# Performance work log

Hardware: AMD Instinct MI355X
Metric: run time of the kernel (lower is better)

## Reference

```python
import jax, jax.numpy as jnp
import numpy as np


def gru_cell(inp, h, wi, wh, bi, bh):
    # torch nn.GRU cell math: gates ordered (r, z, n)
    gi = inp @ wi.T + bi          # [3H]
    gh = h @ wh.T + bh            # [3H]
    ir, iz, inn = jnp.split(gi, 3, axis=-1)
    hr, hz, hn = jnp.split(gh, 3, axis=-1)
    r = jax.nn.sigmoid(ir + hr)
    z = jax.nn.sigmoid(iz + hz)
    n = jnp.tanh(inn + r * hn)
    return (1.0 - z) * n + z * h


def setup_inputs() -> dict:
    key = jax.random.key(0)
    C, L = 1024, 2048  # input_size / hidden_size, sequence length
    ks = jax.random.split(key, 11)
    x = jax.random.normal(ks[0], (1, L, C), jnp.float32)
    # attention: Linear(2C, 1), weight ~ N(0, 0.01), bias = -1 (per module init)
    attn_w = jax.random.normal(ks[1], (1, 2 * C), jnp.float32) * 0.01
    attn_b = jnp.full((1,), -1.0, jnp.float32)
    # GRU default torch init: U(-1/sqrt(H), 1/sqrt(H))
    s = 1.0 / np.sqrt(C).astype(np.float32)
    u = lambda k, shape: jax.random.uniform(k, shape, jnp.float32, -s, s)
    w_ih0 = u(ks[2], (3 * C, C)); w_hh0 = u(ks[3], (3 * C, C))
    b_ih0 = u(ks[4], (3 * C,));   b_hh0 = u(ks[5], (3 * C,))
    w_ih1 = u(ks[6], (3 * C, C)); w_hh1 = u(ks[7], (3 * C, C))
    b_ih1 = u(ks[8], (3 * C,));   b_hh1 = u(ks[9], (3 * C,))
    return {"x": x, "attn_w": attn_w, "attn_b": attn_b,
            "w_ih0": w_ih0, "w_hh0": w_hh0, "b_ih0": b_ih0, "b_hh0": b_hh0,
            "w_ih1": w_ih1, "w_hh1": w_hh1, "b_ih1": b_ih1, "b_hh1": b_hh1,
            "lengths": L}


def reference(x, attn_w, attn_b, w_ih0, w_hh0, b_ih0, b_hh0,
              w_ih1, w_hh1, b_ih1, b_hh1, lengths):
    x0 = x[0]                     # [L, C]; batch must be 1
    L, C = x0.shape
    dt = x.dtype

    def step(carry, _):
        out, h0, h1 = carry       # out: [C], h0/h1: [C]
        # attention: score each timestep against previous output
        concated = jnp.concatenate(
            [jnp.broadcast_to(out, (L, C)), x0], axis=1)  # [L, 2C]
        logits = concated @ attn_w.T + attn_b             # [L, 1]
        a = jax.nn.softmax(logits, axis=0)                # softmax over L
        av = jnp.sum(a * x0, axis=0)                      # [C] context vector
        # 2-layer GRU, one timestep
        h0n = gru_cell(av, h0, w_ih0, w_hh0, b_ih0, b_hh0)
        h1n = gru_cell(h0n, h1, w_ih1, w_hh1, b_ih1, b_hh1)
        return (h1n, h0n, h1n), h1n

    init = (jnp.zeros((C,), dt), jnp.zeros((C,), dt), jnp.zeros((C,), dt))
    (_, h0, h1), outs = jax.lax.scan(step, init, None, length=lengths)
    outputs = outs[None]                                  # [1, L, C]
    previous_state = jnp.stack([h0, h1])[:, None, :]      # [2, 1, C]
    return outputs, previous_state
```

## Files before the change

### kernel.cpp

```cpp
#include <hip/hip_runtime.h>
#include <math.h>

#define CC 1024
#define LL 2048
#define NWG 256
#define NT 256

typedef float f4 __attribute__((ext_vector_type(4)));
typedef unsigned u4 __attribute__((ext_vector_type(4)));

#define H1_BASE 4096
#define PKT_PAR 2048
#define WS_FLAGS 8192
#define WS_REL 16384
#define WS_LOGITS 16448
#define WS_AV (WS_LOGITS + LL)
#define WS_MEMSET_BYTES ((WS_REL + 64) * 4)

__device__ __forceinline__ float aload(const float* p) {
  return __hip_atomic_load(p, __ATOMIC_RELAXED, __HIP_MEMORY_SCOPE_AGENT);
}
__device__ __forceinline__ void astore(float* p, float v) {
  __hip_atomic_store(p, v, __ATOMIC_RELAXED, __HIP_MEMORY_SCOPE_AGENT);
}
__device__ __forceinline__ float sigm(float x) { return 1.0f / (1.0f + __expf(-x)); }
__device__ __forceinline__ float tanh_(float x) { return 2.0f / (1.0f + __expf(-2.0f * x)) - 1.0f; }
__device__ __forceinline__ float dot4(f4 a, f4 b) {
  return fmaf(a.x, b.x, fmaf(a.y, b.y, fmaf(a.z, b.z, a.w * b.w)));
}

__device__ __forceinline__ u4 ld16v(const unsigned* p) {
  u4 r;
  asm volatile("global_load_dwordx4 %0, %1, off sc0 sc1" : "=v"(r) : "v"(p) : "memory");
  return r;
}
__device__ __forceinline__ void vm0() { asm volatile("s_waitcnt vmcnt(0)" ::: "memory"); }

__device__ __forceinline__ void pub8(unsigned* p, unsigned val, unsigned tag) {
  unsigned long long pk = (unsigned long long)val | ((unsigned long long)tag << 32);
  (void)__hip_atomic_exchange((unsigned long long*)p, pk, __ATOMIC_RELAXED,
                              __HIP_MEMORY_SCOPE_AGENT);
}

__device__ __forceinline__ void gbar(unsigned* ws_u, unsigned epoch) {
  __syncthreads();
  if (blockIdx.x == 0) {
    const int i = threadIdx.x;
    if (i > 0 && i < NWG) {
      unsigned* slot = ws_u + WS_FLAGS + i * 32;
      while (__hip_atomic_load(slot, __ATOMIC_RELAXED, __HIP_MEMORY_SCOPE_AGENT) < epoch) {
      }
      (void)__hip_atomic_load(slot, __ATOMIC_ACQUIRE, __HIP_MEMORY_SCOPE_AGENT);
    }
    __syncthreads();
    if (i == 0)
      __hip_atomic_store(ws_u + WS_REL, epoch, __ATOMIC_RELEASE, __HIP_MEMORY_SCOPE_AGENT);
    __syncthreads();
  } else {
    if (threadIdx.x == 0) {
      __hip_atomic_store(ws_u + WS_FLAGS + blockIdx.x * 32, epoch, __ATOMIC_RELEASE,
                         __HIP_MEMORY_SCOPE_AGENT);
      unsigned* rel = ws_u + WS_REL;
      while (__hip_atomic_load(rel, __ATOMIC_RELAXED, __HIP_MEMORY_SCOPE_AGENT) < epoch) {
      }
      (void)__hip_atomic_load(rel, __ATOMIC_ACQUIRE, __HIP_MEMORY_SCOPE_AGENT);
    }
    __syncthreads();
  }
}

#define PIN12                                                                        \
  asm volatile("" : "+v"(Wa[0]), "+v"(Wa[1]), "+v"(Wa[2]), "+v"(Wa[3]), "+v"(Wa[4]), \
                    "+v"(Wa[5]), "+v"(Wa[6]), "+v"(Wa[7]), "+v"(Wa[8]), "+v"(Wa[9]), \
                    "+v"(Wa[10]), "+v"(Wa[11]))

__global__ __launch_bounds__(NT, 1) void decoder_kernel(
    const float* __restrict__ x, const float* __restrict__ attn_w,
    const float* __restrict__ w_ih0, const float* __restrict__ w_hh0,
    const float* __restrict__ b_ih0, const float* __restrict__ b_hh0,
    const float* __restrict__ w_ih1, const float* __restrict__ w_hh1,
    const float* __restrict__ b_ih1, const float* __restrict__ b_hh1,
    float* __restrict__ out, float* __restrict__ ws) {
  const int g = blockIdx.x;
  const int tid = threadIdx.x;
  const int lane = tid & 63;
  const int w = tid >> 6;
  const int eg = 4 * g + w;

  unsigned* ws_u = (unsigned*)ws;

  extern __shared__ float wcb[];
  __shared__ __align__(16) float h0s[CC];
  __shared__ __align__(16) float h1s[CC];
  __shared__ float cgi0[12], cbh0[12], cbh1[12], cbi1[12];
  __shared__ float red[NT];

  {
    const float* w2 = attn_w + CC;
#pragma unroll
    for (int s = 0; s < 2; ++s) {
      int t = 8 * g + 2 * w + s;
      const float* xr = x + (size_t)t * CC;
      float p = 0.f;
#pragma unroll
      for (int k = 0; k < 4; ++k) {
        f4 xa = *(const f4*)(xr + 256 * k + 4 * lane);
        f4 wa = *(const f4*)(w2 + 256 * k + 4 * lane);
        p += dot4(xa, wa);
      }
#pragma unroll
      for (int off = 32; off; off >>= 1) p += __shfl_xor(p, off, 64);
      if (lane == 0) astore(ws + WS_LOGITS + t, p);
    }
  }
  gbar(ws_u, 1);

  {
    float myl[8];
#pragma unroll
    for (int s = 0; s < 8; ++s) myl[s] = aload(ws + WS_LOGITS + tid + 256 * s);
    float lm = myl[0];
#pragma unroll
    for (int s = 1; s < 8; ++s) lm = fmaxf(lm, myl[s]);
    red[tid] = lm;
    __syncthreads();
    for (int stp = 128; stp; stp >>= 1) {
      if (tid < stp) red[tid] = fmaxf(red[tid], red[tid + stp]);
      __syncthreads();
    }
    float m = red[0];
    __syncthreads();
    float myw[8];
    float ls = 0.f;
#pragma unroll
    for (int s = 0; s < 8; ++s) {
      myw[s] = __expf(myl[s] - m);
      ls += myw[s];
    }
    red[tid] = ls;
    __syncthreads();
    for (int stp = 128; stp; stp >>= 1) {
      if (tid < stp) red[tid] += red[tid + stp];
      __syncthreads();
    }
    float invZ = 1.0f / red[0];
    __syncthreads();
    float acc[4] = {0.f, 0.f, 0.f, 0.f};
#pragma unroll
    for (int s = 0; s < 8; ++s) {
      int t = tid + 256 * s;
      f4 xa = *(const f4*)(x + (size_t)t * CC + 4 * g);
      acc[0] = fmaf(myw[s], xa.x, acc[0]);
      acc[1] = fmaf(myw[s], xa.y, acc[1]);
      acc[2] = fmaf(myw[s], xa.z, acc[2]);
      acc[3] = fmaf(myw[s], xa.w, acc[3]);
    }
    for (int i = 0; i < 4; ++i) {
      red[tid] = acc[i];
      __syncthreads();
      for (int stp = 128; stp; stp >>= 1) {
        if (tid < stp) red[tid] += red[tid + stp];
        __syncthreads();
      }
      if (tid == 0) astore(ws + WS_AV + 4 * g + i, red[0] * invZ);
      __syncthreads();
    }
  }
  gbar(ws_u, 2);

#pragma unroll
  for (int i = 0; i < 4; ++i) h0s[4 * tid + i] = aload(ws + WS_AV + 4 * tid + i);
  __syncthreads();
  {
    f4 hc[4];
#pragma unroll
    for (int k = 0; k < 4; ++k) hc[k] = *(const f4*)&h0s[256 * k + 4 * lane];
#pragma unroll
    for (int jj = 0; jj < 3; ++jj) {
      int j = 3 * w + jj;
      int gate = j >> 2, e = j & 3;
      int row = gate * CC + 4 * g + e;
      const float* wr = w_ih0 + (size_t)row * CC;
      float p = 0.f;
#pragma unroll
      for (int k = 0; k < 4; ++k) p += dot4(*(const f4*)(wr + 256 * k + 4 * lane), hc[k]);
#pragma unroll
      for (int off = 32; off; off >>= 1) p += __shfl_xor(p, off, 64);
      if (lane == 0) cgi0[j] = p + b_ih0[row];
    }
  }
  if (tid < 12) {
    int gate = tid >> 2, e = tid & 3;
    int row = gate * CC + 4 * g + e;
    cbh0[tid] = b_hh0[row];
    cbh1[tid] = b_hh1[row];
    cbi1[tid] = b_ih1[row];
  }

  f4 Wa[12];
#pragma unroll
  for (int G = 0; G < 3; ++G) {
    const float* wr = w_hh0 + ((size_t)(G * CC + eg) << 10);
#pragma unroll
    for (int k = 0; k < 4; ++k) Wa[G * 4 + k] = *(const f4*)(wr + 256 * k + 4 * lane);
  }

#pragma unroll
  for (int j = 0; j < 24; ++j) {
    int ww = j / 6, r = j % 6;
    int G = r % 3;
    const float* src = (r < 3 ? w_ih1 : w_hh1) + ((size_t)(G * CC + 4 * g + ww) << 10);
    *(f4*)&wcb[(j << 10) + 4 * tid] = *(const f4*)(src + 4 * tid);
  }
#pragma unroll
  for (int i = 0; i < 4; ++i) {
    h0s[4 * tid + i] = 0.f;
    h1s[4 * tid + i] = 0.f;
  }
  __syncthreads();

  float h0last = 0.f;
  u4 pd0a, pd0b, pd1a, pd1b;
  const float* wr6 = wcb + (w * 6) * 1024;

  for (int tau = 0; tau <= LL; ++tau) {
    PIN12;
    if (tau > 0) {
      const unsigned ut = (unsigned)tau;
      const unsigned* p0 = ws_u + (tau & 1) * PKT_PAR + 8 * tid;
      vm0();
      while (pd0a.y != ut || pd0a.w != ut || pd0b.y != ut || pd0b.w != ut) {
        pd0a = ld16v(p0);
        pd0b = ld16v(p0 + 4);
        vm0();
      }
      h0s[4 * tid + 0] = __uint_as_float(pd0a.x);
      h0s[4 * tid + 1] = __uint_as_float(pd0a.z);
      h0s[4 * tid + 2] = __uint_as_float(pd0b.x);
      h0s[4 * tid + 3] = __uint_as_float(pd0b.z);
      const unsigned* p1 = ws_u + H1_BASE + (tau & 1) * PKT_PAR + 8 * tid;
      pd1a = ld16v(p1);
      pd1b = ld16v(p1 + 4);
    }
    __syncthreads();

    float h0new = 0.f;
    if (tau < LL) {
      f4 hc0[4];
#pragma unroll
      for (int k = 0; k < 4; ++k) hc0[k] = *(const f4*)&h0s[256 * k + 4 * lane];
      float pA[3];
#pragma unroll
      for (int G = 0; G < 3; ++G) {
        float p = 0.f;
#pragma unroll
        for (int k = 0; k < 4; ++k) p += dot4(Wa[G * 4 + k], hc0[k]);
        pA[G] = p;
      }
#pragma unroll
      for (int off = 32; off; off >>= 1) {
#pragma unroll
        for (int i = 0; i < 3; ++i) pA[i] += __shfl_xor(pA[i], off, 64);
      }
      float h0prev = h0s[eg];
      float r0 = sigm(cgi0[w] + pA[0] + cbh0[w]);
      float z0 = sigm(cgi0[4 + w] + pA[1] + cbh0[4 + w]);
      float n0 = tanh_(cgi0[8 + w] + r0 * (pA[2] + cbh0[8 + w]));
      h0new = (1.f - z0) * n0 + z0 * h0prev;
      if (tau == LL - 1) h0last = h0new;
      if (lane == 0)
        pub8(ws_u + ((tau + 1) & 1) * PKT_PAR + 2 * eg, __float_as_uint(h0new),
             (unsigned)(tau + 1));
    }

    if (tau > 0) {
      const unsigned ut = (unsigned)tau;
      const unsigned* p1 = ws_u + H1_BASE + (tau & 1) * PKT_PAR + 8 * tid;
      vm0();
      while (pd1a.y != ut || pd1a.w != ut || pd1b.y != ut || pd1b.w != ut) {
        pd1a = ld16v(p1);
        pd1b = ld16v(p1 + 4);
        vm0();
      }
      h1s[4 * tid + 0] = __uint_as_float(pd1a.x);
      h1s[4 * tid + 1] = __uint_as_float(pd1a.z);
      h1s[4 * tid + 2] = __uint_as_float(pd1b.x);
      h1s[4 * tid + 3] = __uint_as_float(pd1b.z);
    }
    __syncthreads();

    if (tau >= 1) {
      f4 hc0[4], hc1[4];
#pragma unroll
      for (int k = 0; k < 4; ++k) {
        hc0[k] = *(const f4*)&h0s[256 * k + 4 * lane];
        hc1[k] = *(const f4*)&h1s[256 * k + 4 * lane];
      }
      float pC[3], pB[3];
#pragma unroll
      for (int G = 0; G < 3; ++G) {
        float pc = 0.f, pb = 0.f;
#pragma unroll
        for (int k = 0; k < 4; ++k) {
          int off = 256 * k + 4 * lane;
          pc += dot4(*(const f4*)&wr6[G * 1024 + off], hc0[k]);
          pb += dot4(*(const f4*)&wr6[(3 + G) * 1024 + off], hc1[k]);
        }
        pC[G] = pc;
        pB[G] = pb;
      }
#pragma unroll
      for (int off = 32; off; off >>= 1) {
#pragma unroll
        for (int i = 0; i < 3; ++i) {
          pC[i] += __shfl_xor(pC[i], off, 64);
          pB[i] += __shfl_xor(pB[i], off, 64);
        }
      }
      float h1prev = h1s[eg];
      float r1 = sigm(pC[0] + cbi1[w] + pB[0] + cbh1[w]);
      float z1 = sigm(pC[1] + cbi1[4 + w] + pB[1] + cbh1[4 + w]);
      float n1 = tanh_(pC[2] + cbi1[8 + w] + r1 * (pB[2] + cbh1[8 + w]));
      float h1new = (1.f - z1) * n1 + z1 * h1prev;
      if (lane == 0) {
        if (tau < LL)
          pub8(ws_u + H1_BASE + ((tau + 1) & 1) * PKT_PAR + 2 * eg,
               __float_as_uint(h1new), (unsigned)(tau + 1));
        out[(size_t)(tau - 1) * CC + eg] = h1new;
        if (tau == LL) {
          out[(size_t)LL * CC + eg] = h0last;
          out[(size_t)LL * CC + CC + eg] = h1new;
        }
      }
    } else if (lane == 0) {
      pub8(ws_u + H1_BASE + 1 * PKT_PAR + 2 * eg, 0u, 1u);
    }

    if (tau < LL) {
      const unsigned* np = ws_u + ((tau + 1) & 1) * PKT_PAR + 8 * tid;
      pd0a = ld16v(np);
      pd0b = ld16v(np + 4);
    }
    __syncthreads();
  }
}

extern "C" void kernel_launch(void* const* d_in, const int* in_sizes, int n_in,
                              void* d_out, int out_size, void* d_ws, size_t ws_size,
                              hipStream_t stream) {
  const float* x = (const float*)d_in[0];
  const float* attn_w = (const float*)d_in[1];
  const float* w_ih0 = (const float*)d_in[3];
  const float* w_hh0 = (const float*)d_in[4];
  const float* b_ih0 = (const float*)d_in[5];
  const float* b_hh0 = (const float*)d_in[6];
  const float* w_ih1 = (const float*)d_in[7];
  const float* w_hh1 = (const float*)d_in[8];
  const float* b_ih1 = (const float*)d_in[9];
  const float* b_hh1 = (const float*)d_in[10];
  float* out = (float*)d_out;
  float* ws = (float*)d_ws;

  static int attr_set = 0;
  if (!attr_set) {
    hipFuncSetAttribute((const void*)decoder_kernel,
                        hipFuncAttributeMaxDynamicSharedMemorySize, 24 * 1024 * 4);
    attr_set = 1;
  }

  hipMemsetAsync(d_ws, 0, WS_MEMSET_BYTES, stream);

  void* args[] = {&x,     &attn_w, &w_ih0, &w_hh0, &b_ih0, &b_hh0,
                  &w_ih1, &w_hh1,  &b_ih1, &b_hh1, &out,   &ws};
  hipLaunchCooperativeKernel((void*)decoder_kernel, dim3(NWG), dim3(NT), args,
                             24 * 1024 * 4, stream);
}
```

Measured before the change: 7.141 ms.

## Use 64 workgroups of 1024 threads and stream layer-1 weights from global

The persistent cooperative kernel shrinks from 256 workgroups of 256 threads to 64 workgroups of 1024 threads, with 16 hidden elements per workgroup. This cuts the number of agents in the per-step grid-wide handshake, and each thread now polls one 8-byte packet with s_sleep backoff. Layer-1 GRU weights are no longer staged in LDS and are read from global memory (L2) every step. The softmax and context reductions are rewritten with wave shuffles. The risks are higher per-step L2 traffic for the layer-1 weights and longer intra-workgroup __syncthreads across 16 waves.

Result: slower. 23.32 ms (+226.6%).

```diff
diff --git a/kernel.cpp b/kernel.cpp
--- a/kernel.cpp
+++ b/kernel.cpp
@@ -3,18 +3,19 @@
 
 #define CC 1024
 #define LL 2048
-#define NWG 256
-#define NT 256
+#define NWG 64
+#define NT 1024
+#define ELPW 16
 
 typedef float f4 __attribute__((ext_vector_type(4)));
-typedef unsigned u4 __attribute__((ext_vector_type(4)));
+typedef unsigned u2v __attribute__((ext_vector_type(2)));
 
 #define H1_BASE 4096
 #define PKT_PAR 2048
 #define WS_FLAGS 8192
-#define WS_REL 16384
-#define WS_LOGITS 16448
-#define WS_AV (WS_LOGITS + LL)
+#define WS_REL 10240
+#define WS_LOGITS 10304
+#define WS_AV 12352
 #define WS_MEMSET_BYTES ((WS_REL + 64) * 4)
 
 __device__ __forceinline__ float aload(const float* p) {
@@ -29,12 +30,13 @@
   return fmaf(a.x, b.x, fmaf(a.y, b.y, fmaf(a.z, b.z, a.w * b.w)));
 }
 
-__device__ __forceinline__ u4 ld16v(const unsigned* p) {
-  u4 r;
-  asm volatile("global_load_dwordx4 %0, %1, off sc0 sc1" : "=v"(r) : "v"(p) : "memory");
+__device__ __forceinline__ u2v ld8v(const unsigned* p) {
+  u2v r;
+  asm volatile("global_load_dwordx2 %0, %1, off sc0 sc1" : "=v"(r) : "v"(p) : "memory");
   return r;
 }
 __device__ __forceinline__ void vm0() { asm volatile("s_waitcnt vmcnt(0)" ::: "memory"); }
+__device__ __forceinline__ void npause() { asm volatile("s_sleep 1" ::: "memory"); }
 
 __device__ __forceinline__ void pub8(unsigned* p, unsigned val, unsigned tag) {
   unsigned long long pk = (unsigned long long)val | ((unsigned long long)tag << 32);
@@ -85,21 +87,21 @@
   const int tid = threadIdx.x;
   const int lane = tid & 63;
   const int w = tid >> 6;
-  const int eg = 4 * g + w;
+  const int eb = ELPW * g;
+  const int eg = eb + w;
 
   unsigned* ws_u = (unsigned*)ws;
 
-  extern __shared__ float wcb[];
   __shared__ __align__(16) float h0s[CC];
   __shared__ __align__(16) float h1s[CC];
-  __shared__ float cgi0[12], cbh0[12], cbh1[12], cbi1[12];
   __shared__ float red[NT];
+  __shared__ float cgi0[48], cbh0[48], cbh1[48], cbi1[48];
 
   {
     const float* w2 = attn_w + CC;
 #pragma unroll
     for (int s = 0; s < 2; ++s) {
-      int t = 8 * g + 2 * w + s;
+      int t = 32 * g + 2 * w + s;
       const float* xr = x + (size_t)t * CC;
       float p = 0.f;
 #pragma unroll
@@ -116,60 +118,67 @@
   gbar(ws_u, 1);
 
   {
-    float myl[8];
-#pragma unroll
-    for (int s = 0; s < 8; ++s) myl[s] = aload(ws + WS_LOGITS + tid + 256 * s);
-    float lm = myl[0];
-#pragma unroll
-    for (int s = 1; s < 8; ++s) lm = fmaxf(lm, myl[s]);
-    red[tid] = lm;
-    __syncthreads();
-    for (int stp = 128; stp; stp >>= 1) {
-      if (tid < stp) red[tid] = fmaxf(red[tid], red[tid + stp]);
-      __syncthreads();
-    }
+    float myl[2];
+#pragma unroll
+    for (int s = 0; s < 2; ++s) myl[s] = aload(ws + WS_LOGITS + tid + 1024 * s);
+    float lm = fmaxf(myl[0], myl[1]);
+#pragma unroll
+    for (int off = 32; off; off >>= 1) lm = fmaxf(lm, __shfl_xor(lm, off, 64));
+    if (lane == 0) red[w] = lm;
+    __syncthreads();
     float m = red[0];
-    __syncthreads();
-    float myw[8];
-    float ls = 0.f;
-#pragma unroll
-    for (int s = 0; s < 8; ++s) {
-      myw[s] = __expf(myl[s] - m);
-      ls += myw[s];
-    }
-    red[tid] = ls;
-    __syncthreads();
-    for (int stp = 128; stp; stp >>= 1) {
-      if (tid < stp) red[tid] += red[tid + stp];
-      __syncthreads();
-    }
-    float invZ = 1.0f / red[0];
-    __syncthreads();
-    float acc[4] = {0.f, 0.f, 0.f, 0.f};
-#pragma unroll
-    for (int s = 0; s < 8; ++s) {
-      int t = tid + 256 * s;
-      f4 xa = *(const f4*)(x + (size_t)t * CC + 4 * g);
-      acc[0] = fmaf(myw[s], xa.x, acc[0]);
-      acc[1] = fmaf(myw[s], xa.y, acc[1]);
-      acc[2] = fmaf(myw[s], xa.z, acc[2]);
-      acc[3] = fmaf(myw[s], xa.w, acc[3]);
-    }
-    for (int i = 0; i < 4; ++i) {
-      red[tid] = acc[i];
-      __syncthreads();
-      for (int stp = 128; stp; stp >>= 1) {
-        if (tid < stp) red[tid] += red[tid + stp];
-        __syncthreads();
-      }
-      if (tid == 0) astore(ws + WS_AV + 4 * g + i, red[0] * invZ);
-      __syncthreads();
+#pragma unroll
+    for (int i = 1; i < 16; ++i) m = fmaxf(m, red[i]);
+    float myw[2];
+    myw[0] = __expf(myl[0] - m);
+    myw[1] = __expf(myl[1] - m);
+    float ls = myw[0] + myw[1];
+#pragma unroll
+    for (int off = 32; off; off >>= 1) ls += __shfl_xor(ls, off, 64);
+    __syncthreads();
+    if (lane == 0) red[16 + w] = ls;
+    __syncthreads();
+    float Z = 0.f;
+#pragma unroll
+    for (int i = 0; i < 16; ++i) Z += red[16 + i];
+    float invZ = 1.0f / Z;
+    float acc[16];
+#pragma unroll
+    for (int c = 0; c < 16; ++c) acc[c] = 0.f;
+#pragma unroll
+    for (int s = 0; s < 2; ++s) {
+      int t = tid + 1024 * s;
+      const float* xr = x + (size_t)t * CC + eb;
+#pragma unroll
+      for (int q = 0; q < 4; ++q) {
+        f4 xa = *(const f4*)(xr + 4 * q);
+        acc[4 * q + 0] = fmaf(myw[s], xa.x, acc[4 * q + 0]);
+        acc[4 * q + 1] = fmaf(myw[s], xa.y, acc[4 * q + 1]);
+        acc[4 * q + 2] = fmaf(myw[s], xa.z, acc[4 * q + 2]);
+        acc[4 * q + 3] = fmaf(myw[s], xa.w, acc[4 * q + 3]);
+      }
+    }
+#pragma unroll
+    for (int c = 0; c < 16; ++c) {
+#pragma unroll
+      for (int off = 32; off; off >>= 1) acc[c] += __shfl_xor(acc[c], off, 64);
+    }
+    __syncthreads();
+    if (lane == 0) {
+#pragma unroll
+      for (int c = 0; c < 16; ++c) red[256 + w * 16 + c] = acc[c];
+    }
+    __syncthreads();
+    if (tid < 16) {
+      float s = 0.f;
+#pragma unroll
+      for (int ww = 0; ww < 16; ++ww) s += red[256 + ww * 16 + tid];
+      astore(ws + WS_AV + eb + tid, s * invZ);
     }
   }
   gbar(ws_u, 2);
 
-#pragma unroll
-  for (int i = 0; i < 4; ++i) h0s[4 * tid + i] = aload(ws + WS_AV + 4 * tid + i);
+  h0s[tid] = aload(ws + WS_AV + tid);
   __syncthreads();
   {
     f4 hc[4];
@@ -178,8 +187,8 @@
 #pragma unroll
     for (int jj = 0; jj < 3; ++jj) {
       int j = 3 * w + jj;
-      int gate = j >> 2, e = j & 3;
-      int row = gate * CC + 4 * g + e;
+      int gate = j >> 4, e = j & 15;
+      int row = gate * CC + eb + e;
       const float* wr = w_ih0 + (size_t)row * CC;
       float p = 0.f;
 #pragma unroll
@@ -189,9 +198,9 @@
       if (lane == 0) cgi0[j] = p + b_ih0[row];
     }
   }
-  if (tid < 12) {
-    int gate = tid >> 2, e = tid & 3;
-    int row = gate * CC + 4 * g + e;
+  if (tid < 48) {
+    int gate = tid >> 4, e = tid & 15;
+    int row = gate * CC + eb + e;
     cbh0[tid] = b_hh0[row];
     cbh1[tid] = b_hh1[row];
     cbi1[tid] = b_ih1[row];
@@ -204,43 +213,33 @@
 #pragma unroll
     for (int k = 0; k < 4; ++k) Wa[G * 4 + k] = *(const f4*)(wr + 256 * k + 4 * lane);
   }
-
-#pragma unroll
-  for (int j = 0; j < 24; ++j) {
-    int ww = j / 6, r = j % 6;
-    int G = r % 3;
-    const float* src = (r < 3 ? w_ih1 : w_hh1) + ((size_t)(G * CC + 4 * g + ww) << 10);
-    *(f4*)&wcb[(j << 10) + 4 * tid] = *(const f4*)(src + 4 * tid);
-  }
-#pragma unroll
-  for (int i = 0; i < 4; ++i) {
-    h0s[4 * tid + i] = 0.f;
-    h1s[4 * tid + i] = 0.f;
-  }
+  const float* wc0 = w_ih1 + ((size_t)(0 * CC + eg) << 10) + 4 * lane;
+  const float* wc1 = w_ih1 + ((size_t)(1 * CC + eg) << 10) + 4 * lane;
+  const float* wc2 = w_ih1 + ((size_t)(2 * CC + eg) << 10) + 4 * lane;
+  const float* wb0 = w_hh1 + ((size_t)(0 * CC + eg) << 10) + 4 * lane;
+  const float* wb1 = w_hh1 + ((size_t)(1 * CC + eg) << 10) + 4 * lane;
+  const float* wb2 = w_hh1 + ((size_t)(2 * CC + eg) << 10) + 4 * lane;
+
+  h0s[tid] = 0.f;
+  h1s[tid] = 0.f;
   __syncthreads();
 
   float h0last = 0.f;
-  u4 pd0a, pd0b, pd1a, pd1b;
-  const float* wr6 = wcb + (w * 6) * 1024;
+  u2v pd0, pd1;
 
   for (int tau = 0; tau <= LL; ++tau) {
     PIN12;
     if (tau > 0) {
       const unsigned ut = (unsigned)tau;
-      const unsigned* p0 = ws_u + (tau & 1) * PKT_PAR + 8 * tid;
+      const unsigned* p0 = ws_u + (tau & 1) * PKT_PAR + 2 * tid;
       vm0();
-      while (pd0a.y != ut || pd0a.w != ut || pd0b.y != ut || pd0b.w != ut) {
-        pd0a = ld16v(p0);
-        pd0b = ld16v(p0 + 4);
+      while (pd0.y != ut) {
+        npause();
+        pd0 = ld8v(p0);
         vm0();
       }
-      h0s[4 * tid + 0] = __uint_as_float(pd0a.x);
-      h0s[4 * tid + 1] = __uint_as_float(pd0a.z);
-      h0s[4 * tid + 2] = __uint_as_float(pd0b.x);
-      h0s[4 * tid + 3] = __uint_as_float(pd0b.z);
-      const unsigned* p1 = ws_u + H1_BASE + (tau & 1) * PKT_PAR + 8 * tid;
-      pd1a = ld16v(p1);
-      pd1b = ld16v(p1 + 4);
+      h0s[tid] = __uint_as_float(pd0.x);
+      pd1 = ld8v(ws_u + H1_BASE + (tau & 1) * PKT_PAR + 2 * tid);
     }
     __syncthreads();
 
@@ -264,8 +263,8 @@
       }
       float h0prev = h0s[eg];
       float r0 = sigm(cgi0[w] + pA[0] + cbh0[w]);
-      float z0 = sigm(cgi0[4 + w] + pA[1] + cbh0[4 + w]);
-      float n0 = tanh_(cgi0[8 + w] + r0 * (pA[2] + cbh0[8 + w]));
+      float z0 = sigm(cgi0[16 + w] + pA[1] + cbh0[16 + w]);
+      float n0 = tanh_(cgi0[32 + w] + r0 * (pA[2] + cbh0[32 + w]));
       h0new = (1.f - z0) * n0 + z0 * h0prev;
       if (tau == LL - 1) h0last = h0new;
       if (lane == 0)
@@ -275,17 +274,14 @@
 
     if (tau > 0) {
       const unsigned ut = (unsigned)tau;
-      const unsigned* p1 = ws_u + H1_BASE + (tau & 1) * PKT_PAR + 8 * tid;
+      const unsigned* p1 = ws_u + H1_BASE + (tau & 1) * PKT_PAR + 2 * tid;
       vm0();
-      while (pd1a.y != ut || pd1a.w != ut || pd1b.y != ut || pd1b.w != ut) {
-        pd1a = ld16v(p1);
-        pd1b = ld16v(p1 + 4);
+      while (pd1.y != ut) {
+        npause();
+        pd1 = ld8v(p1);
         vm0();
       }
-      h1s[4 * tid + 0] = __uint_as_float(pd1a.x);
-      h1s[4 * tid + 1] = __uint_as_float(pd1a.z);
-      h1s[4 * tid + 2] = __uint_as_float(pd1b.x);
-      h1s[4 * tid + 3] = __uint_as_float(pd1b.z);
+      h1s[tid] = __uint_as_float(pd1.x);
     }
     __syncthreads();
 
@@ -297,17 +293,20 @@
         hc1[k] = *(const f4*)&h1s[256 * k + 4 * lane];
       }
       float pC[3], pB[3];
-#pragma unroll
-      for (int G = 0; G < 3; ++G) {
-        float pc = 0.f, pb = 0.f;
+      {
+        float c0 = 0.f, c1 = 0.f, c2 = 0.f, b0 = 0.f, b1 = 0.f, b2 = 0.f;
 #pragma unroll
         for (int k = 0; k < 4; ++k) {
-          int off = 256 * k + 4 * lane;
-          pc += dot4(*(const f4*)&wr6[G * 1024 + off], hc0[k]);
-          pb += dot4(*(const f4*)&wr6[(3 + G) * 1024 + off], hc1[k]);
+          int o = 256 * k;
+          c0 += dot4(*(const f4*)(wc0 + o), hc0[k]);
+          c1 += dot4(*(const f4*)(wc1 + o), hc0[k]);
+          c2 += dot4(*(const f4*)(wc2 + o), hc0[k]);
+          b0 += dot4(*(const f4*)(wb0 + o), hc1[k]);
+          b1 += dot4(*(const f4*)(wb1 + o), hc1[k]);
+          b2 += dot4(*(const f4*)(wb2 + o), hc1[k]);
         }
-        pC[G] = pc;
-        pB[G] = pb;
+        pC[0] = c0; pC[1] = c1; pC[2] = c2;
+        pB[0] = b0; pB[1] = b1; pB[2] = b2;
       }
 #pragma unroll
       for (int off = 32; off; off >>= 1) {
@@ -319,8 +318,8 @@
       }
       float h1prev = h1s[eg];
       float r1 = sigm(pC[0] + cbi1[w] + pB[0] + cbh1[w]);
-      float z1 = sigm(pC[1] + cbi1[4 + w] + pB[1] + cbh1[4 + w]);
-      float n1 = tanh_(pC[2] + cbi1[8 + w] + r1 * (pB[2] + cbh1[8 + w]));
+      float z1 = sigm(pC[1] + cbi1[16 + w] + pB[1] + cbh1[16 + w]);
+      float n1 = tanh_(pC[2] + cbi1[32 + w] + r1 * (pB[2] + cbh1[32 + w]));
       float h1new = (1.f - z1) * n1 + z1 * h1prev;
       if (lane == 0) {
         if (tau < LL)
@@ -336,11 +335,7 @@
       pub8(ws_u + H1_BASE + 1 * PKT_PAR + 2 * eg, 0u, 1u);
     }
 
-    if (tau < LL) {
-      const unsigned* np = ws_u + ((tau + 1) & 1) * PKT_PAR + 8 * tid;
-      pd0a = ld16v(np);
-      pd0b = ld16v(np + 4);
-    }
+    if (tau < LL) pd0 = ld8v(ws_u + ((tau + 1) & 1) * PKT_PAR + 2 * tid);
     __syncthreads();
   }
 }
@@ -361,17 +356,10 @@
   float* out = (float*)d_out;
   float* ws = (float*)d_ws;
 
-  static int attr_set = 0;
-  if (!attr_set) {
-    hipFuncSetAttribute((const void*)decoder_kernel,
-                        hipFuncAttributeMaxDynamicSharedMemorySize, 24 * 1024 * 4);
-    attr_set = 1;
-  }
-
   hipMemsetAsync(d_ws, 0, WS_MEMSET_BYTES, stream);
 
   void* args[] = {&x,     &attn_w, &w_ih0, &w_hh0, &b_ih0, &b_hh0,
                   &w_ih1, &w_hh1,  &b_ih1, &b_hh1, &out,   &ws};
-  hipLaunchCooperativeKernel((void*)decoder_kernel, dim3(NWG), dim3(NT), args,
-                             24 * 1024 * 4, stream);
-}
+  hipLaunchCooperativeKernel((void*)decoder_kernel, dim3(NWG), dim3(NT), args, 0,
+                             stream);
+}
```

## Double-buffer hidden-state LDS, drop trailing barrier, prefetch next h0 packet earlier

Applied to the files above, without the earlier changes.

Adds a second LDS buffer for h0 and h1 indexed by timestep parity, which makes the end-of-step __syncthreads unnecessary, so it is removed. The prefetch of the next layer-0 packet is moved to before the layer-1 matvec and re-issued partway through if its tags are stale. Atomic 64-bit exchanges are replaced with plain dwordx2 stores carrying sc0 sc1 bits, and the first poll waits with vmcnt(1) instead of vmcnt(0). This removes one barrier and some atomic latency per step on the recurrent critical path, but the correctness of the relaxed stores and the shorter wait now depends on how the hardware orders these memory operations.

After: 8.574 ms. 20.1% more time.

```diff
diff --git a/kernel.cpp b/kernel.cpp
--- a/kernel.cpp
+++ b/kernel.cpp
@@ -8,6 +8,7 @@
 
 typedef float f4 __attribute__((ext_vector_type(4)));
 typedef unsigned u4 __attribute__((ext_vector_type(4)));
+typedef unsigned u2v __attribute__((ext_vector_type(2)));
 
 #define H1_BASE 4096
 #define PKT_PAR 2048
@@ -35,11 +36,12 @@
   return r;
 }
 __device__ __forceinline__ void vm0() { asm volatile("s_waitcnt vmcnt(0)" ::: "memory"); }
-
-__device__ __forceinline__ void pub8(unsigned* p, unsigned val, unsigned tag) {
-  unsigned long long pk = (unsigned long long)val | ((unsigned long long)tag << 32);
-  (void)__hip_atomic_exchange((unsigned long long*)p, pk, __ATOMIC_RELAXED,
-                              __HIP_MEMORY_SCOPE_AGENT);
+__device__ __forceinline__ void vm1() { asm volatile("s_waitcnt vmcnt(1)" ::: "memory"); }
+__device__ __forceinline__ void st8u(unsigned* p, unsigned val, unsigned tag) {
+  u2v v;
+  v.x = val;
+  v.y = tag;
+  asm volatile("global_store_dwordx2 %0, %1, off sc0 sc1" ::"v"(p), "v"(v) : "memory");
 }
 
 __device__ __forceinline__ void gbar(unsigned* ws_u, unsigned epoch) {
@@ -90,8 +92,8 @@
   unsigned* ws_u = (unsigned*)ws;
 
   extern __shared__ float wcb[];
-  __shared__ __align__(16) float h0s[CC];
-  __shared__ __align__(16) float h1s[CC];
+  __shared__ __align__(16) float h0s[2][CC];
+  __shared__ __align__(16) float h1s[2][CC];
   __shared__ float cgi0[12], cbh0[12], cbh1[12], cbi1[12];
   __shared__ float red[NT];
 
@@ -169,12 +171,12 @@
   gbar(ws_u, 2);
 
 #pragma unroll
-  for (int i = 0; i < 4; ++i) h0s[4 * tid + i] = aload(ws + WS_AV + 4 * tid + i);
+  for (int i = 0; i < 4; ++i) h0s[0][4 * tid + i] = aload(ws + WS_AV + 4 * tid + i);
   __syncthreads();
   {
     f4 hc[4];
 #pragma unroll
-    for (int k = 0; k < 4; ++k) hc[k] = *(const f4*)&h0s[256 * k + 4 * lane];
+    for (int k = 0; k < 4; ++k) hc[k] = *(const f4*)&h0s[0][256 * k + 4 * lane];
 #pragma unroll
     for (int jj = 0; jj < 3; ++jj) {
       int j = 3 * w + jj;
@@ -196,6 +198,7 @@
     cbh1[tid] = b_hh1[row];
     cbi1[tid] = b_ih1[row];
   }
+  __syncthreads();
 
   f4 Wa[12];
 #pragma unroll
@@ -214,8 +217,10 @@
   }
 #pragma unroll
   for (int i = 0; i < 4; ++i) {
-    h0s[4 * tid + i] = 0.f;
-    h1s[4 * tid + i] = 0.f;
+    h0s[0][4 * tid + i] = 0.f;
+    h0s[1][4 * tid + i] = 0.f;
+    h1s[0][4 * tid + i] = 0.f;
+    h1s[1][4 * tid + i] = 0.f;
   }
   __syncthreads();
 
@@ -225,20 +230,21 @@
 
   for (int tau = 0; tau <= LL; ++tau) {
     PIN12;
+    const int p = tau & 1;
     if (tau > 0) {
       const unsigned ut = (unsigned)tau;
-      const unsigned* p0 = ws_u + (tau & 1) * PKT_PAR + 8 * tid;
+      const unsigned* p0 = ws_u + p * PKT_PAR + 8 * tid;
       vm0();
       while (pd0a.y != ut || pd0a.w != ut || pd0b.y != ut || pd0b.w != ut) {
         pd0a = ld16v(p0);
         pd0b = ld16v(p0 + 4);
         vm0();
       }
-      h0s[4 * tid + 0] = __uint_as_float(pd0a.x);
-      h0s[4 * tid + 1] = __uint_as_float(pd0a.z);
-      h0s[4 * tid + 2] = __uint_as_float(pd0b.x);
-      h0s[4 * tid + 3] = __uint_as_float(pd0b.z);
-      const unsigned* p1 = ws_u + H1_BASE + (tau & 1) * PKT_PAR + 8 * tid;
+      h0s[p][4 * tid + 0] = __uint_as_float(pd0a.x);
+      h0s[p][4 * tid + 1] = __uint_as_float(pd0a.z);
+      h0s[p][4 * tid + 2] = __uint_as_float(pd0b.x);
+      h0s[p][4 * tid + 3] = __uint_as_float(pd0b.z);
+      const unsigned* p1 = ws_u + H1_BASE + p * PKT_PAR + 8 * tid;
       pd1a = ld16v(p1);
       pd1b = ld16v(p1 + 4);
     }
@@ -248,65 +254,83 @@
     if (tau < LL) {
       f4 hc0[4];
 #pragma unroll
-      for (int k = 0; k < 4; ++k) hc0[k] = *(const f4*)&h0s[256 * k + 4 * lane];
+      for (int k = 0; k < 4; ++k) hc0[k] = *(const f4*)&h0s[p][256 * k + 4 * lane];
       float pA[3];
 #pragma unroll
       for (int G = 0; G < 3; ++G) {
-        float p = 0.f;
-#pragma unroll
-        for (int k = 0; k < 4; ++k) p += dot4(Wa[G * 4 + k], hc0[k]);
-        pA[G] = p;
+        float pp = 0.f;
+#pragma unroll
+        for (int k = 0; k < 4; ++k) pp += dot4(Wa[G * 4 + k], hc0[k]);
+        pA[G] = pp;
       }
 #pragma unroll
       for (int off = 32; off; off >>= 1) {
 #pragma unroll
         for (int i = 0; i < 3; ++i) pA[i] += __shfl_xor(pA[i], off, 64);
       }
-      float h0prev = h0s[eg];
+      float h0prev = h0s[p][eg];
       float r0 = sigm(cgi0[w] + pA[0] + cbh0[w]);
       float z0 = sigm(cgi0[4 + w] + pA[1] + cbh0[4 + w]);
       float n0 = tanh_(cgi0[8 + w] + r0 * (pA[2] + cbh0[8 + w]));
       h0new = (1.f - z0) * n0 + z0 * h0prev;
       if (tau == LL - 1) h0last = h0new;
       if (lane == 0)
-        pub8(ws_u + ((tau + 1) & 1) * PKT_PAR + 2 * eg, __float_as_uint(h0new),
+        st8u(ws_u + (p ^ 1) * PKT_PAR + 2 * eg, __float_as_uint(h0new),
              (unsigned)(tau + 1));
     }
 
     if (tau > 0) {
       const unsigned ut = (unsigned)tau;
-      const unsigned* p1 = ws_u + H1_BASE + (tau & 1) * PKT_PAR + 8 * tid;
-      vm0();
+      const unsigned* p1 = ws_u + H1_BASE + p * PKT_PAR + 8 * tid;
+      vm1();
       while (pd1a.y != ut || pd1a.w != ut || pd1b.y != ut || pd1b.w != ut) {
         pd1a = ld16v(p1);
         pd1b = ld16v(p1 + 4);
         vm0();
       }
-      h1s[4 * tid + 0] = __uint_as_float(pd1a.x);
-      h1s[4 * tid + 1] = __uint_as_float(pd1a.z);
-      h1s[4 * tid + 2] = __uint_as_float(pd1b.x);
-      h1s[4 * tid + 3] = __uint_as_float(pd1b.z);
-    }
-    __syncthreads();
-
+      h1s[p][4 * tid + 0] = __uint_as_float(pd1a.x);
+      h1s[p][4 * tid + 1] = __uint_as_float(pd1a.z);
+      h1s[p][4 * tid + 2] = __uint_as_float(pd1b.x);
+      h1s[p][4 * tid + 3] = __uint_as_float(pd1b.z);
+    }
+    __syncthreads();
+
+    const unsigned* np = ws_u + (p ^ 1) * PKT_PAR + 8 * tid;
+    if (tau < LL) {
+      pd0a = ld16v(np);
+      pd0b = ld16v(np + 4);
+    }
     if (tau >= 1) {
       f4 hc0[4], hc1[4];
 #pragma unroll
       for (int k = 0; k < 4; ++k) {
-        hc0[k] = *(const f4*)&h0s[256 * k + 4 * lane];
-        hc1[k] = *(const f4*)&h1s[256 * k + 4 * lane];
-      }
-      float pC[3], pB[3];
+        hc0[k] = *(const f4*)&h0s[p][256 * k + 4 * lane];
+        hc1[k] = *(const f4*)&h1s[p][256 * k + 4 * lane];
+      }
+      float pC[3];
 #pragma unroll
       for (int G = 0; G < 3; ++G) {
-        float pc = 0.f, pb = 0.f;
-#pragma unroll
-        for (int k = 0; k < 4; ++k) {
-          int off = 256 * k + 4 * lane;
-          pc += dot4(*(const f4*)&wr6[G * 1024 + off], hc0[k]);
-          pb += dot4(*(const f4*)&wr6[(3 + G) * 1024 + off], hc1[k]);
+        float pc = 0.f;
+#pragma unroll
+        for (int k = 0; k < 4; ++k)
+          pc += dot4(*(const f4*)&wr6[G * 1024 + 256 * k + 4 * lane], hc0[k]);
+        pC[G] = pc;
+      }
+      if (tau < LL) {
+        const unsigned nt_ = (unsigned)(tau + 1);
+        vm0();
+        if (pd0a.y != nt_ || pd0a.w != nt_ || pd0b.y != nt_ || pd0b.w != nt_) {
+          pd0a = ld16v(np);
+          pd0b = ld16v(np + 4);
         }
-        pC[G] = pc;
+      }
+      float pB[3];
+#pragma unroll
+      for (int G = 0; G < 3; ++G) {
+        float pb = 0.f;
+#pragma unroll
+        for (int k = 0; k < 4; ++k)
+          pb += dot4(*(const f4*)&wr6[(3 + G) * 1024 + 256 * k + 4 * lane], hc1[k]);
         pB[G] = pb;
       }
 #pragma unroll
@@ -317,15 +341,15 @@
           pB[i] += __shfl_xor(pB[i], off, 64);
         }
       }
-      float h1prev = h1s[eg];
+      float h1prev = h1s[p][eg];
       float r1 = sigm(pC[0] + cbi1[w] + pB[0] + cbh1[w]);
       float z1 = sigm(pC[1] + cbi1[4 + w] + pB[1] + cbh1[4 + w]);
       float n1 = tanh_(pC[2] + cbi1[8 + w] + r1 * (pB[2] + cbh1[8 + w]));
       float h1new = (1.f - z1) * n1 + z1 * h1prev;
       if (lane == 0) {
         if (tau < LL)
-          pub8(ws_u + H1_BASE + ((tau + 1) & 1) * PKT_PAR + 2 * eg,
-               __float_as_uint(h1new), (unsigned)(tau + 1));
+          st8u(ws_u + H1_BASE + (p ^ 1) * PKT_PAR + 2 * eg, __float_as_uint(h1new),
+               (unsigned)(tau + 1));
         out[(size_t)(tau - 1) * CC + eg] = h1new;
         if (tau == LL) {
           out[(size_t)LL * CC + eg] = h0last;
@@ -333,15 +357,8 @@
         }
       }
     } else if (lane == 0) {
-      pub8(ws_u + H1_BASE + 1 * PKT_PAR + 2 * eg, 0u, 1u);
-    }
-
-    if (tau < LL) {
-      const unsigned* np = ws_u + ((tau + 1) & 1) * PKT_PAR + 8 * tid;
-      pd0a = ld16v(np);
-      pd0b = ld16v(np + 4);
-    }
-    __syncthreads();
+      st8u(ws_u + H1_BASE + 1 * PKT_PAR + 2 * eg, 0u, 1u);
+    }
   }
 }
 
```
